# Optimization experiments

Measured on AMD Instinct MI355X. Metric: run time of the kernel, lower is better.

Reference implementation:

```python
import jax, jax.numpy as jnp
import numpy as np

_EPSILON = 1e-06


def _allocation(usage):
    """Freeness-based allocation: sort usage, exclusive cumprod, scatter back.

    usage: [B, M] in [0, 1]. Returns allocation weights [B, M].
    """
    usage = _EPSILON + (1.0 - _EPSILON) * usage
    nonusage = 1.0 - usage
    m = usage.shape[-1]
    sorted_nonusage, indices = jax.lax.top_k(nonusage, k=m)  # descending nonusage = ascending usage
    sorted_usage = 1.0 - sorted_nonusage
    # exclusive cumulative product along the sorted memory axis
    prod_sorted_usage = jnp.concatenate(
        [jnp.ones_like(sorted_usage[:, :1]),
         jnp.cumprod(sorted_usage, axis=1)[:, :-1]], axis=1)
    sorted_allocation = sorted_nonusage * prod_sorted_usage
    # invert the permutation and gather back to original slot order
    inverse_indices = jnp.argsort(indices, axis=1)
    return jnp.take_along_axis(sorted_allocation, inverse_indices, axis=1)


def _updated_usage(write_weights, free_gate, read_weights, prev_usage):
    """Freeness.__call__: usage after write then after read/free. [B, M]."""
    ww = jax.lax.stop_gradient(write_weights)
    # usage after write: increase toward 1 at written slots
    write_w = 1.0 - jnp.prod(1.0 - ww, axis=1)          # [B, M]
    usage = prev_usage + (1.0 - prev_usage) * write_w
    # usage after read: decrease where free_gate*read_weights is high
    free_read = free_gate[:, :, None] * read_weights      # [B, R, M]
    phi = jnp.prod(1.0 - free_read, axis=1)               # [B, M]
    return usage * phi


def _write_allocation_weights(usage, write_gates, num_writes):
    """Per-write-head allocation weights. Returns [B, num_writes, M]."""
    wg = write_gates[:, :, None]                          # [B, W, 1]
    allocs = []
    for i in range(num_writes):  # small fixed head count; sequential by construction
        a = _allocation(usage)
        allocs.append(a)
        usage = usage + (1.0 - usage) * wg[:, i, :] * a
    return jnp.stack(allocs, axis=1)


def setup_inputs() -> dict:
    key = jax.random.key(0)
    ks = jax.random.split(key, 5)
    B, W, R, M = 512, 4, 8, 16384
    return {
        "write_weights": jax.random.uniform(ks[0], (B, W, M), dtype=jnp.float32),
        "free_gate": jax.random.uniform(ks[1], (B, R), dtype=jnp.float32),
        "read_weights": jax.random.uniform(ks[2], (B, R, M), dtype=jnp.float32),
        "prev_usage": jax.random.uniform(ks[3], (B, M), dtype=jnp.float32),
        "write_gates": jax.random.uniform(ks[4], (B, W), dtype=jnp.float32),
        "num_writes": W,
    }


def reference(write_weights, free_gate, read_weights, prev_usage, write_gates, num_writes):
    usage = _updated_usage(write_weights, free_gate, read_weights, prev_usage)
    alloc = _write_allocation_weights(usage, write_gates, num_writes)
    return usage, alloc
```

## Files before the change

kernel.cpp:

```cpp
#include <hip/hip_runtime.h>
#include <stdint.h>

typedef unsigned long long u64;
typedef unsigned int u32;

#define NBINS 512
#define CAP 512
#define LOG_CUT (-64.0f)
#define LOG_SCALE 20.0f
#define NT 1024

template <int TW, int TR>
__global__ __launch_bounds__(NT, 8)
void fused_kernel(const float* __restrict__ ww,
                  const float* __restrict__ fg,
                  const float* __restrict__ rw,
                  const float* __restrict__ prev,
                  const float* __restrict__ wgt,
                  float* __restrict__ out_usage,
                  float* __restrict__ out_alloc,
                  int B, int W, int R, int M)
{
    __shared__ u64   keyS[CAP];
    __shared__ float logS[CAP];
    __shared__ u32   hC[NBINS];
    __shared__ u32   tc[16];
    __shared__ float twv[16];
    __shared__ int   misc[4];
    extern __shared__ float uS[];

    const int Wl = TW > 0 ? TW : W;
    const int Rl = TR > 0 ? TR : R;
    const int b = blockIdx.x;
    const int t = threadIdx.x;
    const int lane = t & 63;
    const int wid = t >> 6;

    const float C1 = (float)(1.0 - 1e-6);
    const float CE = 1e-6f;

    {
        const size_t rowOff = (size_t)b * M;
        float frs[TR > 0 ? TR : 8];
        #pragma unroll
        for (int r = 0; r < Rl; ++r) frs[r] = fg[(size_t)b * Rl + r];

        const float4 z = make_float4(0.f, 0.f, 0.f, 0.f);
        for (int m = t * 4; m < M; m += NT * 4) {
            const float4 pv = *(const float4*)(prev + rowOff + m);
            float pr0 = 1.f, pr1 = 1.f, pr2 = 1.f, pr3 = 1.f;
            #pragma unroll
            for (int w = 0; w < Wl; ++w) {
                const float4 a = *(const float4*)(ww + ((size_t)b * Wl + w) * M + m);
                pr0 *= (1.0f - a.x); pr1 *= (1.0f - a.y);
                pr2 *= (1.0f - a.z); pr3 *= (1.0f - a.w);
            }
            float u0 = pv.x + (1.0f - pv.x) * (1.0f - pr0);
            float u1 = pv.y + (1.0f - pv.y) * (1.0f - pr1);
            float u2 = pv.z + (1.0f - pv.z) * (1.0f - pr2);
            float u3 = pv.w + (1.0f - pv.w) * (1.0f - pr3);
            float f0 = 1.f, f1 = 1.f, f2 = 1.f, f3 = 1.f;
            #pragma unroll
            for (int r = 0; r < Rl; ++r) {
                const float fr = frs[r];
                const float4 a = *(const float4*)(rw + ((size_t)b * Rl + r) * M + m);
                f0 *= (1.0f - fr * a.x); f1 *= (1.0f - fr * a.y);
                f2 *= (1.0f - fr * a.z); f3 *= (1.0f - fr * a.w);
            }
            float4 uo;
            uo.x = u0 * f0; uo.y = u1 * f1; uo.z = u2 * f2; uo.w = u3 * f3;
            *(float4*)(uS + m) = uo;
            *(float4*)(out_usage + rowOff + m) = uo;
            #pragma unroll
            for (int w = 0; w < Wl; ++w)
                *(float4*)(out_alloc + ((size_t)b * Wl + w) * M + m) = z;
        }
    }

    for (int i = 0; i < Wl; ++i) {
        const float wgi = wgt[(size_t)b * Wl + i];
        float* orow = out_alloc + ((size_t)b * Wl + i) * M;

        if (t < NBINS) hC[t] = 0u;
        if (t == 0) { misc[0] = 0; misc[1] = -1; misc[2] = NBINS; }
        __syncthreads();

        for (int x = t * 4; x < M; x += NT * 4) {
            const float4 uu = *(const float4*)(uS + x);
            const float ua[4] = {uu.x, uu.y, uu.z, uu.w};
            #pragma unroll
            for (int j = 0; j < 4; ++j) {
                const float ue = CE + C1 * ua[j];
                const float lg = __log2f(ue);
                int bkt = (int)(-lg * LOG_SCALE);
                bkt = bkt < 0 ? 0 : (bkt > NBINS - 1 ? NBINS - 1 : bkt);
                atomicAdd(&hC[bkt], 1u);
            }
        }
        __syncthreads();

        {
            const bool act = (t < NBINS);
            u32 sc = 0; float sw = 0.f; int x = 0;
            if (act) {
                x = NBINS - 1 - t;
                const u32 c = hC[x];
                sc = c;
                sw = -(float)x * (1.0f / LOG_SCALE) * (float)c;
                #pragma unroll
                for (int off = 1; off < 64; off <<= 1) {
                    const u32  oc = __shfl_up(sc, off);
                    const float ow = __shfl_up(sw, off);
                    if (lane >= off) { sc += oc; sw += ow; }
                }
                if (lane == 63) { tc[wid] = sc; twv[wid] = sw; }
            }
            __syncthreads();
            if (act) {
                u32 ac = 0; float aw = 0.f;
                for (int q = 0; q < wid; ++q) { ac += tc[q]; aw += twv[q]; }
                sc += ac; sw += aw;
                if (sw <= LOG_CUT) atomicMax(&misc[1], x);
                if (sc <= (u32)CAP) atomicMin(&misc[2], x);
            }
        }
        __syncthreads();
        const int xs = misc[1];
        const int xc = misc[2];
        const int cut = (xs > xc) ? xs : xc;

        for (int x = t; x < M; x += NT) {
            const float u = uS[x];
            const float ue = CE + C1 * u;
            const float lg = __log2f(ue);
            int bkt = (int)(-lg * LOG_SCALE);
            bkt = bkt < 0 ? 0 : (bkt > NBINS - 1 ? NBINS - 1 : bkt);
            const bool pred = (bkt >= cut) && (cut < NBINS);
            const u64 mask = __ballot(pred);
            const int cnt = __popcll(mask);
            if (cnt) {
                int base = 0;
                if (lane == 0) base = atomicAdd(&misc[0], cnt);
                base = __shfl(base, 0);
                if (pred) {
                    const int pos = base + __popcll(mask & ((1ull << lane) - 1));
                    if (pos < CAP) {
                        const float nn = 1.0f - ue;
                        keyS[pos] = (((u64)(~__float_as_uint(nn))) << 14) | (u64)(u32)x;
                        logS[pos] = lg;
                    }
                }
            }
        }
        __syncthreads();
        int K = misc[0]; if (K > CAP) K = CAP;

        if (t < K) {
            const u64 mykey = keyS[t];
            float S = 0.0f;
            #pragma unroll 4
            for (int k = 0; k < K; ++k) {
                const u64 kk = keyS[k];
                const float lg = logS[k];
                if (kk < mykey) S += lg;
            }
            const float nn = __uint_as_float(~((u32)(mykey >> 14)));
            const int idx = (int)(mykey & 0x3FFFull);
            const float al = nn * __builtin_exp2f(S);
            if (al != 0.0f) {
                orow[idx] = al;
                const float u0v = uS[idx];
                uS[idx] = u0v + ((1.0f - u0v) * wgi) * al;
            }
        }
        __syncthreads();
    }
}

extern "C" void kernel_launch(void* const* d_in, const int* in_sizes, int n_in,
                              void* d_out, int out_size, void* d_ws, size_t ws_size,
                              hipStream_t stream) {
    const float* ww   = (const float*)d_in[0];
    const float* fg   = (const float*)d_in[1];
    const float* rw   = (const float*)d_in[2];
    const float* prev = (const float*)d_in[3];
    const float* wgt  = (const float*)d_in[4];
    const int BWM = in_sizes[0];
    const int BR  = in_sizes[1];
    const int BM  = in_sizes[3];
    const int BW  = in_sizes[4];
    const int M = BWM / BW;
    const int B = BM / M;
    const int W = BW / B;
    const int R = BR / B;

    float* out_usage = (float*)d_out;
    float* out_alloc = out_usage + (size_t)BM;

    const size_t smem = (size_t)M * sizeof(float);
    if (W == 4 && R == 8) {
        hipLaunchKernelGGL((fused_kernel<4, 8>), dim3(B), dim3(NT), smem, stream,
                           ww, fg, rw, prev, wgt, out_usage, out_alloc, B, W, R, M);
    } else {
        hipLaunchKernelGGL((fused_kernel<0, 0>), dim3(B), dim3(NT), smem, stream,
                           ww, fg, rw, prev, wgt, out_usage, out_alloc, B, W, R, M);
    }
}
```

Before: 157.0 us.

## Build histogram once with bit-based buckets and update incrementally per write head

Replaces the log2-based bucketing with an integer bucket derived from the float bits of the nonusage value, and precomputes a per-bucket log upper bound table. The histogram is built once during the usage pass and then adjusted only for the few slots whose usage changes after each write head, instead of being rebuilt over all M slots per head. Output stores become nontemporal. This removes W-1 full histogram passes and many log evaluations, at the cost of more complex bucket bounds that must stay conservative for the cutoff to be correct.

```diff
diff --git a/kernel.cpp b/kernel.cpp
--- a/kernel.cpp
+++ b/kernel.cpp
@@ -3,12 +3,28 @@
 
 typedef unsigned long long u64;
 typedef unsigned int u32;
+typedef float f32x4 __attribute__((ext_vector_type(4)));
 
 #define NBINS 512
 #define CAP 512
 #define LOG_CUT (-64.0f)
-#define LOG_SCALE 20.0f
 #define NT 1024
+
+__device__ __forceinline__ int bucket_of(u32 nnbits) {
+    u32 d = 0x3F800000u - nnbits;
+    if (d == 0u) d = 1u;
+    const int e = 31 - __builtin_clz(d);
+    const u32 sub = (e >= 4) ? ((d >> (e - 4)) & 15u) : ((d << (4 - e)) & 15u);
+    int v = (e << 4) | (int)sub;
+    if (v > NBINS - 1) v = NBINS - 1;
+    return (NBINS - 1) - v;
+}
+
+__device__ __forceinline__ void nt_store4(float* p, float4 v) {
+    f32x4 nv;
+    nv.x = v.x; nv.y = v.y; nv.z = v.z; nv.w = v.w;
+    __builtin_nontemporal_store(nv, (f32x4*)p);
+}
 
 template <int TW, int TR>
 __global__ __launch_bounds__(NT, 8)
@@ -24,6 +40,7 @@
     __shared__ u64   keyS[CAP];
     __shared__ float logS[CAP];
     __shared__ u32   hC[NBINS];
+    __shared__ float mB[NBINS];
     __shared__ u32   tc[16];
     __shared__ float twv[16];
     __shared__ int   misc[4];
@@ -39,6 +56,21 @@
     const float C1 = (float)(1.0 - 1e-6);
     const float CE = 1e-6f;
 
+    if (t < NBINS) {
+        hC[t] = 0u;
+        const int v = NBINS - 1 - t;
+        const int e = v >> 4;
+        const u32 sub = (u32)(v & 15);
+        const int sh = e >= 4 ? e - 4 : 0;
+        u64 dhi64 = ((u64)(17u + sub) << sh) + 1u;
+        u32 dhi = dhi64 > 0x3F800000ull ? 0x3F800000u : (u32)dhi64;
+        const float nnlo = __uint_as_float(0x3F800000u - dhi);
+        float ueub = 1.0f - nnlo;
+        ueub = ueub < 1e-38f ? 1e-38f : (ueub > 0.9999999f ? 0.9999999f : ueub);
+        mB[t] = __log2f(ueub);
+    }
+    __syncthreads();
+
     {
         const size_t rowOff = (size_t)b * M;
         float frs[TR > 0 ? TR : 8];
@@ -70,10 +102,16 @@
             float4 uo;
             uo.x = u0 * f0; uo.y = u1 * f1; uo.z = u2 * f2; uo.w = u3 * f3;
             *(float4*)(uS + m) = uo;
-            *(float4*)(out_usage + rowOff + m) = uo;
+            nt_store4(out_usage + rowOff + m, uo);
             #pragma unroll
             for (int w = 0; w < Wl; ++w)
-                *(float4*)(out_alloc + ((size_t)b * Wl + w) * M + m) = z;
+                nt_store4(out_alloc + ((size_t)b * Wl + w) * M + m, z);
+            const float ua[4] = {uo.x, uo.y, uo.z, uo.w};
+            #pragma unroll
+            for (int j = 0; j < 4; ++j) {
+                const float nn = 1.0f - (CE + C1 * ua[j]);
+                atomicAdd(&hC[bucket_of(__float_as_uint(nn))], 1u);
+            }
         }
     }
 
@@ -81,22 +119,7 @@
         const float wgi = wgt[(size_t)b * Wl + i];
         float* orow = out_alloc + ((size_t)b * Wl + i) * M;
 
-        if (t < NBINS) hC[t] = 0u;
         if (t == 0) { misc[0] = 0; misc[1] = -1; misc[2] = NBINS; }
-        __syncthreads();
-
-        for (int x = t * 4; x < M; x += NT * 4) {
-            const float4 uu = *(const float4*)(uS + x);
-            const float ua[4] = {uu.x, uu.y, uu.z, uu.w};
-            #pragma unroll
-            for (int j = 0; j < 4; ++j) {
-                const float ue = CE + C1 * ua[j];
-                const float lg = __log2f(ue);
-                int bkt = (int)(-lg * LOG_SCALE);
-                bkt = bkt < 0 ? 0 : (bkt > NBINS - 1 ? NBINS - 1 : bkt);
-                atomicAdd(&hC[bkt], 1u);
-            }
-        }
         __syncthreads();
 
         {
@@ -106,7 +129,7 @@
                 x = NBINS - 1 - t;
                 const u32 c = hC[x];
                 sc = c;
-                sw = -(float)x * (1.0f / LOG_SCALE) * (float)c;
+                sw = mB[x] * (float)c;
                 #pragma unroll
                 for (int off = 1; off < 64; off <<= 1) {
                     const u32  oc = __shfl_up(sc, off);
@@ -132,9 +155,8 @@
         for (int x = t; x < M; x += NT) {
             const float u = uS[x];
             const float ue = CE + C1 * u;
-            const float lg = __log2f(ue);
-            int bkt = (int)(-lg * LOG_SCALE);
-            bkt = bkt < 0 ? 0 : (bkt > NBINS - 1 ? NBINS - 1 : bkt);
+            const float nn = 1.0f - ue;
+            const int bkt = bucket_of(__float_as_uint(nn));
             const bool pred = (bkt >= cut) && (cut < NBINS);
             const u64 mask = __ballot(pred);
             const int cnt = __popcll(mask);
@@ -145,9 +167,8 @@
                 if (pred) {
                     const int pos = base + __popcll(mask & ((1ull << lane) - 1));
                     if (pos < CAP) {
-                        const float nn = 1.0f - ue;
                         keyS[pos] = (((u64)(~__float_as_uint(nn))) << 14) | (u64)(u32)x;
-                        logS[pos] = lg;
+                        logS[pos] = __log2f(ue);
                     }
                 }
             }
@@ -164,13 +185,24 @@
                 const float lg = logS[k];
                 if (kk < mykey) S += lg;
             }
-            const float nn = __uint_as_float(~((u32)(mykey >> 14)));
+            const u32 nnbits = ~((u32)(mykey >> 14));
+            const float nn = __uint_as_float(nnbits);
             const int idx = (int)(mykey & 0x3FFFull);
             const float al = nn * __builtin_exp2f(S);
             if (al != 0.0f) {
                 orow[idx] = al;
-                const float u0v = uS[idx];
-                uS[idx] = u0v + ((1.0f - u0v) * wgi) * al;
+                if (i + 1 < Wl) {
+                    const float u0v = uS[idx];
+                    const float unew = u0v + ((1.0f - u0v) * wgi) * al;
+                    uS[idx] = unew;
+                    const int bold = bucket_of(nnbits);
+                    const float nn2 = 1.0f - (CE + C1 * unew);
+                    const int bnew = bucket_of(__float_as_uint(nn2));
+                    if (bnew != bold) {
+                        atomicSub(&hC[bold], 1u);
+                        atomicAdd(&hC[bnew], 1u);
+                    }
+                }
             }
         }
         __syncthreads();
```

Result: faster. 149.0 us (-5.1%).
